# Kernel optimization log

Hardware: AMD Instinct MI355X
Metric: run time of the kernel (lower is better)

## Reference

```python
import jax, jax.numpy as jnp
import numpy as np

N_NODES = 100000
N_EDGES = 3200000
NEG_SLOPE = 0.2


def setup_inputs() -> dict:
    key = jax.random.key(0)
    k = jax.random.split(key, 7)
    feat = jax.random.normal(k[0], (N_NODES, 256), dtype=jnp.float32)
    W_fc = jax.random.normal(k[1], (64, 256), dtype=jnp.float32) * 0.05
    attn_l = jax.random.normal(k[2], (4, 16), dtype=jnp.float32) * 0.1
    attn_r = jax.random.normal(k[3], (4, 16), dtype=jnp.float32) * 0.1
    W_res = jax.random.normal(k[4], (64, 256), dtype=jnp.float32) * 0.05
    src = jax.random.randint(k[5], (N_EDGES,), 0, N_NODES, dtype=jnp.int32)
    dst = jax.random.randint(k[6], (N_EDGES,), 0, N_NODES, dtype=jnp.int32)
    return {"feat": feat, "W_fc": W_fc, "attn_l": attn_l, "attn_r": attn_r,
            "W_res": W_res, "src": src, "dst": dst}


def reference(feat, W_fc, attn_l, attn_r, W_res, src, dst):
    N = feat.shape[0]
    H, D = attn_l.shape
    # Linear projection -> per-head features [N, H, D]
    feat_src = (feat @ W_fc.T).reshape(N, H, D)
    # Per-node attention logits [N, H]
    el = jnp.einsum('nhd,hd->nh', feat_src, attn_l)
    er = jnp.einsum('nhd,hd->nh', feat_src, attn_r)
    # fused_gat: per-edge leaky-relu score, edge softmax over dst, scatter-sum
    e = jax.nn.leaky_relu(el[src] + er[dst], negative_slope=NEG_SLOPE)  # [E, H]
    emax = jax.ops.segment_max(e, dst, num_segments=N)  # [N, H]
    emax = jnp.where(jnp.isfinite(emax), emax, 0.0)  # zero-degree safety
    ee = jnp.exp(e - emax[dst])  # [E, H]
    denom = jax.ops.segment_sum(ee, dst, num_segments=N)  # [N, H]
    alpha = ee / jnp.maximum(denom[dst], 1e-20)  # [E, H]
    # weighted aggregation of source features -> [N, H, D]
    rst = jax.ops.segment_sum(alpha[:, :, None] * feat_src[src], dst,
                              num_segments=N)
    # residual connection (res_fc always present in this module)
    resval = (feat @ W_res.T).reshape(N, H, D)
    return rst + resval
```

## Files before the change

### kernel.cpp

```cpp
#include <hip/hip_runtime.h>
#include <hip/hip_bf16.h>


#define F_IN 256
#define O_OUT 64
#define NEG_SLOPE 0.2f

using frag_ab = __attribute__((ext_vector_type(8))) short;
using frag_cd = __attribute__((ext_vector_type(4))) float;

__device__ __forceinline__ float lrelu(float x) {
    return x >= 0.0f ? x : NEG_SLOPE * x;
}

__device__ __forceinline__ unsigned short f2bf(float f) {
    unsigned int u = __float_as_uint(f);
    unsigned int r = (u + 0x7fffu + ((u >> 16) & 1u)) >> 16;
    return (unsigned short)r;
}
__device__ __forceinline__ float bflo(unsigned int p) {
    return __uint_as_float(p << 16);
}
__device__ __forceinline__ float bfhi(unsigned int p) {
    return __uint_as_float(p & 0xffff0000u);
}

__global__ __launch_bounds__(256) void wprep_kernel(
    const float* __restrict__ Wfc, const float* __restrict__ Wres,
    unsigned short* __restrict__ Bf)
{
    int tid = blockIdx.x * 256 + threadIdx.x;
    int ct = tid >> 9;
    int lane = tid & 63;
    int ks = (tid >> 6) & 7;
    int col = ct * 16 + (lane & 15);
    int kbase = ks * 32 + (lane >> 4) * 8;
    const float* srcW = (col < 64) ? (Wfc + (size_t)col * 256 + kbase)
                                   : (Wres + (size_t)(col - 64) * 256 + kbase);
    unsigned short* dstp = Bf + (size_t)tid * 8;
#pragma unroll
    for (int i = 0; i < 8; ++i) dstp[i] = f2bf(srcW[i]);
}

__global__ __launch_bounds__(256) void proj_mfma_kernel(
    const float* __restrict__ feat, const unsigned short* __restrict__ Bf,
    const float* __restrict__ attn_l, const float* __restrict__ attn_r,
    unsigned short* __restrict__ fsb, float* __restrict__ el,
    float* __restrict__ er, float* __restrict__ out,
    int* __restrict__ counts_zero, float* __restrict__ denom_zero, int N)
{
    __shared__ __align__(16) unsigned short sA[64 * 280];
    const int t = threadIdx.x;
    const int lane = t & 63;
    const int w = t >> 6;
    const int n0 = blockIdx.x * 64;
    if (n0 >= N) return;

    frag_ab bfrag[2][8];
    {
        const unsigned short* bp = Bf + (size_t)lane * 8;
#pragma unroll
        for (int j = 0; j < 2; ++j)
#pragma unroll
            for (int ks = 0; ks < 8; ++ks)
                bfrag[j][ks] = *(const frag_ab*)(bp + (size_t)((2 * w + j) * 8 + ks) * 512);
    }

    if (counts_zero && t < 64 && n0 + t < N) counts_zero[n0 + t] = 0;
    if (denom_zero && n0 * 4 + t < N * 4) denom_zero[n0 * 4 + t] = 0.0f;

    for (int i = 0; i < 8; ++i) {
        int f = i * 256 + t;
        int row = f >> 5, c8 = f & 31;
        int n = n0 + row;
        float4 v0 = make_float4(0.f, 0.f, 0.f, 0.f), v1 = v0;
        if (n < N) {
            const float4* p = (const float4*)(feat + (size_t)n * F_IN + c8 * 8);
            v0 = p[0]; v1 = p[1];
        }
        frag_ab pack;
        pack[0] = (short)f2bf(v0.x); pack[1] = (short)f2bf(v0.y);
        pack[2] = (short)f2bf(v0.z); pack[3] = (short)f2bf(v0.w);
        pack[4] = (short)f2bf(v1.x); pack[5] = (short)f2bf(v1.y);
        pack[6] = (short)f2bf(v1.z); pack[7] = (short)f2bf(v1.w);
        *(frag_ab*)(&sA[row * 280 + c8 * 8]) = pack;
    }
    __syncthreads();

    frag_cd acc[4][2];
#pragma unroll
    for (int rt = 0; rt < 4; ++rt)
#pragma unroll
        for (int j = 0; j < 2; ++j)
            acc[rt][j] = (frag_cd){0.f, 0.f, 0.f, 0.f};

#pragma unroll
    for (int ks = 0; ks < 8; ++ks) {
        frag_ab af[4];
#pragma unroll
        for (int rt = 0; rt < 4; ++rt) {
            int row = rt * 16 + (lane & 15);
            int c8 = ks * 4 + (lane >> 4);
            af[rt] = *(const frag_ab*)(&sA[row * 280 + c8 * 8]);
        }
#pragma unroll
        for (int rt = 0; rt < 4; ++rt)
#pragma unroll
            for (int j = 0; j < 2; ++j)
                acc[rt][j] = __builtin_amdgcn_mfma_f32_16x16x32_bf16(
                    af[rt], bfrag[j][ks], acc[rt][j], 0, 0, 0);
    }

    const int colq = lane & 15;
    const int quad = lane >> 4;
    if (w < 2) {
#pragma unroll
        for (int j = 0; j < 2; ++j) {
            int h = 2 * w + j;
            float al = attn_l[h * 16 + colq];
            float ar = attn_r[h * 16 + colq];
#pragma unroll
            for (int rt = 0; rt < 4; ++rt)
#pragma unroll
                for (int r = 0; r < 4; ++r) {
                    int node = n0 + rt * 16 + quad * 4 + r;
                    float v = acc[rt][j][r];
                    if (node < N) fsb[(size_t)node * O_OUT + h * 16 + colq] = f2bf(v);
                    float pl = v * al, pr = v * ar;
                    pl += __shfl_xor(pl, 1); pr += __shfl_xor(pr, 1);
                    pl += __shfl_xor(pl, 2); pr += __shfl_xor(pr, 2);
                    pl += __shfl_xor(pl, 4); pr += __shfl_xor(pr, 4);
                    pl += __shfl_xor(pl, 8); pr += __shfl_xor(pr, 8);
                    if (colq == 0 && node < N) {
                        el[(size_t)node * 4 + h] = pl;
                        er[(size_t)node * 4 + h] = pr;
                    }
                }
        }
    } else {
#pragma unroll
        for (int j = 0; j < 2; ++j) {
            int cb = 32 * (w - 2) + 16 * j;
#pragma unroll
            for (int rt = 0; rt < 4; ++rt)
#pragma unroll
                for (int r = 0; r < 4; ++r) {
                    int node = n0 + rt * 16 + quad * 4 + r;
                    if (node < N)
                        out[(size_t)node * O_OUT + cb + colq] = acc[rt][j][r];
                }
        }
    }
}

__global__ __launch_bounds__(256) void hist_kernel(
    const int* __restrict__ dst, int* __restrict__ counts,
    int* __restrict__ rank, int E)
{
    int e = blockIdx.x * 256 + threadIdx.x;
    if (e < E) rank[e] = atomicAdd(&counts[dst[e]], 1);
}

__global__ __launch_bounds__(256) void scan_block_kernel(
    const int* __restrict__ counts, int* __restrict__ rowptr,
    int* __restrict__ bsums, int N)
{
    int t = threadIdx.x;
    int base = blockIdx.x * 1024 + t * 4;
    int c0 = 0, c1 = 0, c2 = 0, c3 = 0;
    if (base + 3 < N) {
        int4 v = *(const int4*)(counts + base);
        c0 = v.x; c1 = v.y; c2 = v.z; c3 = v.w;
    } else {
        if (base     < N) c0 = counts[base];
        if (base + 1 < N) c1 = counts[base + 1];
        if (base + 2 < N) c2 = counts[base + 2];
        if (base + 3 < N) c3 = counts[base + 3];
    }
    int tsum = c0 + c1 + c2 + c3;
    int inc = tsum;
    int lane = t & 63, wid = t >> 6;
#pragma unroll
    for (int o = 1; o < 64; o <<= 1) {
        int v = __shfl_up(inc, o);
        if (lane >= o) inc += v;
    }
    __shared__ int wsum[4];
    if (lane == 63) wsum[wid] = inc;
    __syncthreads();
    int woff = 0;
#pragma unroll
    for (int w = 0; w < 4; ++w)
        if (w < wid) woff += wsum[w];
    int excl = woff + inc - tsum;
    int e0 = excl, e1 = excl + c0, e2 = e1 + c1, e3 = e2 + c2;
    if (base + 3 < N) {
        *(int4*)(rowptr + base) = make_int4(e0, e1, e2, e3);
    } else {
        if (base     < N) rowptr[base]     = e0;
        if (base + 1 < N) rowptr[base + 1] = e1;
        if (base + 2 < N) rowptr[base + 2] = e2;
        if (base + 3 < N) rowptr[base + 3] = e3;
    }
    if (t == 255) bsums[blockIdx.x] = wsum[0] + wsum[1] + wsum[2] + wsum[3];
}

__global__ void scan_bsums_kernel(int* __restrict__ bsums, int nb)
{
    int lane = threadIdx.x;
    int carry = 0;
    for (int c = 0; c * 64 < nb; ++c) {
        int i = c * 64 + lane;
        int v = (i < nb) ? bsums[i] : 0;
        int inc = v;
#pragma unroll
        for (int o = 1; o < 64; o <<= 1) {
            int u = __shfl_up(inc, o);
            if (lane >= o) inc += u;
        }
        if (i < nb) bsums[i] = carry + inc - v;
        carry += __shfl(inc, 63);
    }
}

__global__ __launch_bounds__(256) void scan_final_kernel(
    int* __restrict__ rowptr, const int* __restrict__ bsums, int N, int E)
{
    int i = blockIdx.x * 256 + threadIdx.x;
    if (i < N) rowptr[i] = rowptr[i] + bsums[i >> 10];
    if (i == 0) rowptr[N] = E;
}

__global__ __launch_bounds__(256) void scatter_kernel(
    const int* __restrict__ src, const int* __restrict__ dst,
    const int* __restrict__ rank, const int* __restrict__ rowptr,
    int* __restrict__ sorted_src, int E)
{
    int e = blockIdx.x * 256 + threadIdx.x;
    if (e >= E) return;
    sorted_src[rowptr[dst[e]] + rank[e]] = src[e];
}

__global__ __launch_bounds__(256) void agg_csr_kernel(
    const int* __restrict__ rowptr, const int* __restrict__ srt,
    const unsigned short* __restrict__ fsb, const float* __restrict__ el,
    const float* __restrict__ er, float* __restrict__ out, int N)
{
    int d = blockIdx.x * 4 + (threadIdx.x >> 6);
    if (d >= N) return;
    const int lane = threadIdx.x & 63;
    const int half = lane >> 5;
    const int c = lane & 31;
    const int h = c >> 3;
    const int k0 = rowptr[d], k1 = rowptr[d + 1];
    const float erh = er[(size_t)d * 4 + h];
    float a0 = 0.f, a1 = 0.f, den = 0.f;

    int kb = k0;
    for (; kb + 8 <= k1; kb += 8) {
        int s0 = srt[kb + half];
        int s1 = srt[kb + 2 + half];
        int s2 = srt[kb + 4 + half];
        int s3 = srt[kb + 6 + half];
        float e0 = el[(size_t)s0 * 4 + h];
        float e1 = el[(size_t)s1 * 4 + h];
        float e2 = el[(size_t)s2 * 4 + h];
        float e3 = el[(size_t)s3 * 4 + h];
        unsigned int f0 = *(const unsigned int*)(fsb + (size_t)s0 * O_OUT + 2 * c);
        unsigned int f1 = *(const unsigned int*)(fsb + (size_t)s1 * O_OUT + 2 * c);
        unsigned int f2 = *(const unsigned int*)(fsb + (size_t)s2 * O_OUT + 2 * c);
        unsigned int f3 = *(const unsigned int*)(fsb + (size_t)s3 * O_OUT + 2 * c);
        float w0 = __expf(lrelu(e0 + erh));
        float w1 = __expf(lrelu(e1 + erh));
        float w2 = __expf(lrelu(e2 + erh));
        float w3 = __expf(lrelu(e3 + erh));
        a0 += w0 * bflo(f0); a1 += w0 * bfhi(f0); den += w0;
        a0 += w1 * bflo(f1); a1 += w1 * bfhi(f1); den += w1;
        a0 += w2 * bflo(f2); a1 += w2 * bfhi(f2); den += w2;
        a0 += w3 * bflo(f3); a1 += w3 * bfhi(f3); den += w3;
    }
    for (; kb < k1; kb += 2) {
        int ki = kb + half;
        if (ki < k1) {
            int s = srt[ki];
            float w = __expf(lrelu(el[(size_t)s * 4 + h] + erh));
            unsigned int f = *(const unsigned int*)(fsb + (size_t)s * O_OUT + 2 * c);
            a0 += w * bflo(f); a1 += w * bfhi(f); den += w;
        }
    }
    a0 += __shfl_xor(a0, 32);
    a1 += __shfl_xor(a1, 32);
    den += __shfl_xor(den, 32);
    if (half == 0) {
        float inv = 1.0f / fmaxf(den, 1e-20f);
        float2* po = (float2*)(out + (size_t)d * O_OUT + 2 * c);
        float2 o = *po;
        o.x += a0 * inv;
        o.y += a1 * inv;
        *po = o;
    }
}

__global__ __launch_bounds__(256) void edge_sum_kernel(
    const int* __restrict__ src, const int* __restrict__ dst,
    const float* __restrict__ el, const float* __restrict__ er,
    float* __restrict__ denom, int E)
{
    int e = blockIdx.x * 256 + threadIdx.x;
    if (e >= E) return;
    int s = src[e], d = dst[e];
    float4 l4 = ((const float4*)el)[s];
    float4 r4 = ((const float4*)er)[d];
    unsafeAtomicAdd(&denom[(size_t)d * 4 + 0], __expf(lrelu(l4.x + r4.x)));
    unsafeAtomicAdd(&denom[(size_t)d * 4 + 1], __expf(lrelu(l4.y + r4.y)));
    unsafeAtomicAdd(&denom[(size_t)d * 4 + 2], __expf(lrelu(l4.z + r4.z)));
    unsafeAtomicAdd(&denom[(size_t)d * 4 + 3], __expf(lrelu(l4.w + r4.w)));
}

__global__ __launch_bounds__(256) void agg_atomic_kernel(
    const int* __restrict__ src, const int* __restrict__ dst,
    const unsigned short* __restrict__ fsb, const float* __restrict__ el,
    const float* __restrict__ er, const float* __restrict__ denom,
    float* __restrict__ out, int E)
{
    const int lane = threadIdx.x & 63;
    const int wid = threadIdx.x >> 6;
    int e = blockIdx.x * 4 + wid;
    if (e >= E) return;
    int s = src[e], d = dst[e];
    int h = lane >> 4;
    float v = __expf(lrelu(el[(size_t)s * 4 + h] + er[(size_t)d * 4 + h]));
    float alpha = v / fmaxf(denom[(size_t)d * 4 + h], 1e-20f);
    float fval = __uint_as_float(((unsigned int)fsb[(size_t)s * O_OUT + lane]) << 16);
    unsafeAtomicAdd(&out[(size_t)d * O_OUT + lane], alpha * fval);
}

extern "C" void kernel_launch(void* const* d_in, const int* in_sizes, int n_in,
                              void* d_out, int out_size, void* d_ws, size_t ws_size,
                              hipStream_t stream) {
    const float* feat   = (const float*)d_in[0];
    const float* Wfc    = (const float*)d_in[1];
    const float* attn_l = (const float*)d_in[2];
    const float* attn_r = (const float*)d_in[3];
    const float* Wres   = (const float*)d_in[4];
    const int*   src    = (const int*)d_in[5];
    const int*   dst    = (const int*)d_in[6];

    const int N = in_sizes[0] / F_IN;
    const int E = in_sizes[5];
    float* out = (float*)d_out;

    float* el     = (float*)d_ws;
    float* er     = el + (size_t)N * 4;
    unsigned short* Bf = (unsigned short*)(er + (size_t)N * 4);
    int*   counts = (int*)(Bf + 32768);
    int*   rowptr = counts + N;
    int*   bsums  = rowptr + N + 4;
    int*   rank   = bsums + 1024;
    int*   sorted_src = rank + E;
    unsigned short* fsb = (unsigned short*)(sorted_src + E);
    size_t need_main = (size_t)((char*)(fsb + (size_t)N * O_OUT) - (char*)d_ws);

    int nproj = (N + 63) / 64;

    if (ws_size >= need_main) {
        wprep_kernel<<<16, 256, 0, stream>>>(Wfc, Wres, Bf);
        proj_mfma_kernel<<<nproj, 256, 0, stream>>>(
            feat, Bf, attn_l, attn_r, fsb, el, er, out, counts, nullptr, N);
        hist_kernel<<<(E + 255) / 256, 256, 0, stream>>>(dst, counts, rank, E);
        int nb = (N + 1023) / 1024;
        scan_block_kernel<<<nb, 256, 0, stream>>>(counts, rowptr, bsums, N);
        scan_bsums_kernel<<<1, 64, 0, stream>>>(bsums, nb);
        scan_final_kernel<<<(N + 255) / 256, 256, 0, stream>>>(rowptr, bsums, N, E);
        scatter_kernel<<<(E + 255) / 256, 256, 0, stream>>>(
            src, dst, rank, rowptr, sorted_src, E);
        agg_csr_kernel<<<(N + 3) / 4, 256, 0, stream>>>(
            rowptr, sorted_src, fsb, el, er, out, N);
    } else {
        float* denom = (float*)counts;
        unsigned short* fsb2 = (unsigned short*)(denom + (size_t)N * 4);
        wprep_kernel<<<16, 256, 0, stream>>>(Wfc, Wres, Bf);
        proj_mfma_kernel<<<nproj, 256, 0, stream>>>(
            feat, Bf, attn_l, attn_r, fsb2, el, er, out, nullptr, denom, N);
        edge_sum_kernel<<<(E + 255) / 256, 256, 0, stream>>>(src, dst, el, er, denom, E);
        agg_atomic_kernel<<<(E + 3) / 4, 256, 0, stream>>>(
            src, dst, fsb2, el, er, denom, out, E);
    }
}
```

Measured before the change: 523.7 us.

## Replace global-atomic CSR build with two-level LDS bucket sort by destination

Swaps the global atomic histogram plus random scatter for a two-pass bucketed counting sort. Edges are first binned by dst>>7 using per-chunk LDS histograms, and the transposed histogram is scanned to place edges in bucket order. A per-bucket kernel then sorts each bucket by the low 7 bits in LDS to produce rowptr and sorted_src. This is meant to cut contended global atomics and scattered writes, at the cost of extra passes, an added packed intermediate array and more launches.

```diff
diff --git a/kernel.cpp b/kernel.cpp
--- a/kernel.cpp
+++ b/kernel.cpp
@@ -5,6 +5,8 @@
 #define F_IN 256
 #define O_OUT 64
 #define NEG_SLOPE 0.2f
+#define CHUNK 16384
+#define RMAX 2048
 
 using frag_ab = __attribute__((ext_vector_type(8))) short;
 using frag_cd = __attribute__((ext_vector_type(4))) float;
@@ -47,7 +49,7 @@
     const float* __restrict__ attn_l, const float* __restrict__ attn_r,
     unsigned short* __restrict__ fsb, float* __restrict__ el,
     float* __restrict__ er, float* __restrict__ out,
-    int* __restrict__ counts_zero, float* __restrict__ denom_zero, int N)
+    float* __restrict__ denom_zero, int N)
 {
     __shared__ __align__(16) unsigned short sA[64 * 280];
     const int t = threadIdx.x;
@@ -66,7 +68,6 @@
                 bfrag[j][ks] = *(const frag_ab*)(bp + (size_t)((2 * w + j) * 8 + ks) * 512);
     }
 
-    if (counts_zero && t < 64 && n0 + t < N) counts_zero[n0 + t] = 0;
     if (denom_zero && n0 * 4 + t < N * 4) denom_zero[n0 * 4 + t] = 0.0f;
 
     for (int i = 0; i < 8; ++i) {
@@ -153,29 +154,37 @@
     }
 }
 
-__global__ __launch_bounds__(256) void hist_kernel(
-    const int* __restrict__ dst, int* __restrict__ counts,
-    int* __restrict__ rank, int E)
-{
-    int e = blockIdx.x * 256 + threadIdx.x;
-    if (e < E) rank[e] = atomicAdd(&counts[dst[e]], 1);
+__global__ __launch_bounds__(256) void bucket_count_kernel(
+    const int* __restrict__ dst, int* __restrict__ histT, int E, int B, int R)
+{
+    __shared__ int h[RMAX];
+    int b = blockIdx.x, t = threadIdx.x;
+    for (int i = t; i < R; i += 256) h[i] = 0;
+    __syncthreads();
+    int base = b * CHUNK;
+    for (int i = t; i < CHUNK; i += 256) {
+        int e = base + i;
+        if (e < E) atomicAdd(&h[dst[e] >> 7], 1);
+    }
+    __syncthreads();
+    for (int i = t; i < R; i += 256) histT[(size_t)i * B + b] = h[i];
 }
 
 __global__ __launch_bounds__(256) void scan_block_kernel(
-    const int* __restrict__ counts, int* __restrict__ rowptr,
-    int* __restrict__ bsums, int N)
+    const int* __restrict__ counts, int* __restrict__ outp,
+    int* __restrict__ bsums, int n)
 {
     int t = threadIdx.x;
     int base = blockIdx.x * 1024 + t * 4;
     int c0 = 0, c1 = 0, c2 = 0, c3 = 0;
-    if (base + 3 < N) {
+    if (base + 3 < n) {
         int4 v = *(const int4*)(counts + base);
         c0 = v.x; c1 = v.y; c2 = v.z; c3 = v.w;
     } else {
-        if (base     < N) c0 = counts[base];
-        if (base + 1 < N) c1 = counts[base + 1];
-        if (base + 2 < N) c2 = counts[base + 2];
-        if (base + 3 < N) c3 = counts[base + 3];
+        if (base     < n) c0 = counts[base];
+        if (base + 1 < n) c1 = counts[base + 1];
+        if (base + 2 < n) c2 = counts[base + 2];
+        if (base + 3 < n) c3 = counts[base + 3];
     }
     int tsum = c0 + c1 + c2 + c3;
     int inc = tsum;
@@ -194,13 +203,13 @@
         if (w < wid) woff += wsum[w];
     int excl = woff + inc - tsum;
     int e0 = excl, e1 = excl + c0, e2 = e1 + c1, e3 = e2 + c2;
-    if (base + 3 < N) {
-        *(int4*)(rowptr + base) = make_int4(e0, e1, e2, e3);
+    if (base + 3 < n) {
+        *(int4*)(outp + base) = make_int4(e0, e1, e2, e3);
     } else {
-        if (base     < N) rowptr[base]     = e0;
-        if (base + 1 < N) rowptr[base + 1] = e1;
-        if (base + 2 < N) rowptr[base + 2] = e2;
-        if (base + 3 < N) rowptr[base + 3] = e3;
+        if (base     < n) outp[base]     = e0;
+        if (base + 1 < n) outp[base + 1] = e1;
+        if (base + 2 < n) outp[base + 2] = e2;
+        if (base + 3 < n) outp[base + 3] = e3;
     }
     if (t == 255) bsums[blockIdx.x] = wsum[0] + wsum[1] + wsum[2] + wsum[3];
 }
@@ -224,21 +233,81 @@
 }
 
 __global__ __launch_bounds__(256) void scan_final_kernel(
-    int* __restrict__ rowptr, const int* __restrict__ bsums, int N, int E)
+    int* __restrict__ outp, const int* __restrict__ bsums, int n, int total)
 {
     int i = blockIdx.x * 256 + threadIdx.x;
-    if (i < N) rowptr[i] = rowptr[i] + bsums[i >> 10];
-    if (i == 0) rowptr[N] = E;
-}
-
-__global__ __launch_bounds__(256) void scatter_kernel(
+    if (i < n) outp[i] = outp[i] + bsums[i >> 10];
+    if (i == 0) outp[n] = total;
+}
+
+__global__ __launch_bounds__(256) void bucket_scatter_kernel(
     const int* __restrict__ src, const int* __restrict__ dst,
-    const int* __restrict__ rank, const int* __restrict__ rowptr,
-    int* __restrict__ sorted_src, int E)
-{
-    int e = blockIdx.x * 256 + threadIdx.x;
-    if (e >= E) return;
-    sorted_src[rowptr[dst[e]] + rank[e]] = src[e];
+    const int* __restrict__ histS, unsigned int* __restrict__ sorted_pk,
+    int E, int B, int R)
+{
+    __shared__ int h[RMAX];
+    __shared__ int basebin[RMAX];
+    int b = blockIdx.x, t = threadIdx.x;
+    for (int i = t; i < R; i += 256) {
+        h[i] = 0;
+        basebin[i] = histS[(size_t)i * B + b];
+    }
+    __syncthreads();
+    int base = b * CHUNK;
+    for (int i = t; i < CHUNK; i += 256) {
+        int e = base + i;
+        if (e < E) {
+            int d = dst[e];
+            int bin = d >> 7;
+            int rk = atomicAdd(&h[bin], 1);
+            sorted_pk[basebin[bin] + rk] =
+                ((unsigned int)src[e] << 7) | (unsigned int)(d & 127);
+        }
+    }
+}
+
+__global__ __launch_bounds__(256) void bucket_build_kernel(
+    const int* __restrict__ histS, const unsigned int* __restrict__ sorted_pk,
+    int* __restrict__ rowptr, int* __restrict__ sorted_src,
+    int N, int E, int B, int R)
+{
+    __shared__ unsigned int buf[8192];
+    __shared__ int hist[128], scn[128], cur[128];
+    int r = blockIdx.x, t = threadIdx.x;
+    int start = histS[(size_t)r * B];
+    int end = (r + 1 < R) ? histS[(size_t)(r + 1) * B] : E;
+    int cnt = end - start;
+    if (t < 128) hist[t] = 0;
+    __syncthreads();
+    bool use_lds = (cnt <= 8192);
+    for (int i = t; i < cnt; i += 256) {
+        unsigned int pk = sorted_pk[start + i];
+        if (use_lds) buf[i] = pk;
+        atomicAdd(&hist[pk & 127], 1);
+    }
+    __syncthreads();
+    if (t < 128) scn[t] = hist[t];
+    __syncthreads();
+    for (int o = 1; o < 128; o <<= 1) {
+        int v = 0;
+        if (t < 128 && t >= o) v = scn[t - o];
+        __syncthreads();
+        if (t < 128) scn[t] += v;
+        __syncthreads();
+    }
+    if (t < 128) {
+        int node = r * 128 + t;
+        if (node < N) rowptr[node] = start + scn[t] - hist[t];
+        cur[t] = 0;
+    }
+    if (r == 0 && t == 0) rowptr[N] = E;
+    __syncthreads();
+    for (int i = t; i < cnt; i += 256) {
+        unsigned int pk = use_lds ? buf[i] : sorted_pk[start + i];
+        int low = pk & 127;
+        int rk = atomicAdd(&cur[low], 1);
+        sorted_src[start + (scn[low] - hist[low]) + rk] = (int)(pk >> 7);
+    }
 }
 
 __global__ __launch_bounds__(256) void agg_csr_kernel(
@@ -350,38 +419,44 @@
     const int E = in_sizes[5];
     float* out = (float*)d_out;
 
+    const int R = (N + 127) >> 7;
+    const int B = (E + CHUNK - 1) / CHUNK;
+    const int nRB = R * B;
+
     float* el     = (float*)d_ws;
     float* er     = el + (size_t)N * 4;
     unsigned short* Bf = (unsigned short*)(er + (size_t)N * 4);
-    int*   counts = (int*)(Bf + 32768);
-    int*   rowptr = counts + N;
-    int*   bsums  = rowptr + N + 4;
-    int*   rank   = bsums + 1024;
-    int*   sorted_src = rank + E;
+    int*   histT  = (int*)(Bf + 32768);
+    int*   histS  = histT + nRB;
+    int*   bsums  = histS + nRB + 8;
+    int*   rowptr = bsums + 1024;
+    unsigned int* sorted_pk = (unsigned int*)(rowptr + N + 4);
+    int*   sorted_src = (int*)(sorted_pk + E);
     unsigned short* fsb = (unsigned short*)(sorted_src + E);
     size_t need_main = (size_t)((char*)(fsb + (size_t)N * O_OUT) - (char*)d_ws);
 
     int nproj = (N + 63) / 64;
 
-    if (ws_size >= need_main) {
+    if (ws_size >= need_main && R <= RMAX) {
         wprep_kernel<<<16, 256, 0, stream>>>(Wfc, Wres, Bf);
         proj_mfma_kernel<<<nproj, 256, 0, stream>>>(
-            feat, Bf, attn_l, attn_r, fsb, el, er, out, counts, nullptr, N);
-        hist_kernel<<<(E + 255) / 256, 256, 0, stream>>>(dst, counts, rank, E);
-        int nb = (N + 1023) / 1024;
-        scan_block_kernel<<<nb, 256, 0, stream>>>(counts, rowptr, bsums, N);
-        scan_bsums_kernel<<<1, 64, 0, stream>>>(bsums, nb);
-        scan_final_kernel<<<(N + 255) / 256, 256, 0, stream>>>(rowptr, bsums, N, E);
-        scatter_kernel<<<(E + 255) / 256, 256, 0, stream>>>(
-            src, dst, rank, rowptr, sorted_src, E);
+            feat, Bf, attn_l, attn_r, fsb, el, er, out, nullptr, N);
+        bucket_count_kernel<<<B, 256, 0, stream>>>(dst, histT, E, B, R);
+        int nsb = (nRB + 1023) / 1024;
+        scan_block_kernel<<<nsb, 256, 0, stream>>>(histT, histS, bsums, nRB);
+        scan_bsums_kernel<<<1, 64, 0, stream>>>(bsums, nsb);
+        scan_final_kernel<<<(nRB + 255) / 256, 256, 0, stream>>>(histS, bsums, nRB, E);
+        bucket_scatter_kernel<<<B, 256, 0, stream>>>(src, dst, histS, sorted_pk, E, B, R);
+        bucket_build_kernel<<<R, 256, 0, stream>>>(
+            histS, sorted_pk, rowptr, sorted_src, N, E, B, R);
         agg_csr_kernel<<<(N + 3) / 4, 256, 0, stream>>>(
             rowptr, sorted_src, fsb, el, er, out, N);
     } else {
-        float* denom = (float*)counts;
+        float* denom = (float*)histT;
         unsigned short* fsb2 = (unsigned short*)(denom + (size_t)N * 4);
         wprep_kernel<<<16, 256, 0, stream>>>(Wfc, Wres, Bf);
         proj_mfma_kernel<<<nproj, 256, 0, stream>>>(
-            feat, Bf, attn_l, attn_r, fsb2, el, er, out, nullptr, denom, N);
+            feat, Bf, attn_l, attn_r, fsb2, el, er, out, denom, N);
         edge_sum_kernel<<<(E + 255) / 256, 256, 0, stream>>>(src, dst, el, er, denom, E);
         agg_atomic_kernel<<<(E + 3) / 4, 256, 0, stream>>>(
             src, dst, fsb2, el, er, denom, out, E);
```

After: 456.7 us. 12.8% less time.
